# Optimization experiments

Hardware: AMD Instinct MI355X
Metric: run time of the kernel (lower is better)

## Reference

```python
import jax, jax.numpy as jnp
import numpy as np

EMBED_DIM = 512
NUM_HEADS = 8
HEAD_DIM = EMBED_DIM // NUM_HEADS
DECAY = 0.95


def setup_inputs() -> dict:
    key = jax.random.key(0)
    ks = jax.random.split(key, 9)
    B, L, D = 2, 4096, EMBED_DIM
    s = 1.0 / np.sqrt(D)
    inp = {
        "x": jax.random.normal(ks[0], (B, L, D), dtype=jnp.float32),
        "Wq": jax.random.normal(ks[1], (D, D), dtype=jnp.float32) * s,
        "bq": jnp.zeros((D,), jnp.float32),
        "Wk": jax.random.normal(ks[2], (D, D), dtype=jnp.float32) * s,
        "bk": jnp.zeros((D,), jnp.float32),
        "Wv": jax.random.normal(ks[3], (D, D), dtype=jnp.float32) * s,
        "bv": jnp.zeros((D,), jnp.float32),
        "Wo": jax.random.normal(ks[4], (D, D), dtype=jnp.float32) * s,
        "bo": jnp.zeros((D,), jnp.float32),
    }
    return inp


def reference(x, Wq, bq, Wk, bk, Wv, bv, Wo, bo):
    B, L, D = x.shape
    H, Hd = NUM_HEADS, HEAD_DIM
    # temporal decay mask: decay_factor ** |i - j|, shape [L, L]
    idx = jnp.arange(L)
    time_diffs = jnp.abs(idx[None, :] - idx[:, None]).astype(x.dtype)
    decay_mask = jnp.power(jnp.asarray(DECAY, x.dtype), time_diffs)  # [L, L]

    def proj(W, b):
        return (x @ W.T + b).reshape(B, L, H, Hd).transpose(0, 2, 1, 3)  # [B,H,L,Hd]

    q = proj(Wq, bq)
    k = proj(Wk, bk)
    v = proj(Wv, bv)

    scale = 1.0 / np.sqrt(Hd)
    scores = jnp.einsum("bhqd,bhkd->bhqk", q, k) * scale  # [B,H,L,L]
    scores = scores * decay_mask  # broadcast over B, H
    probs = jax.nn.softmax(scores, axis=-1)
    out = jnp.einsum("bhqk,bhkd->bhqd", probs, v)  # [B,H,L,Hd]
    out = out.transpose(0, 2, 1, 3).reshape(B, L, D)
    return out @ Wo.T + bo
```

## Files before the change

### kernel.cpp

```cpp
#include <hip/hip_runtime.h>
#include <hip/hip_bf16.h>

#define L_SEQ 4096
#define NB 2
#define NH 8
#define DHEAD 64
#define DMODEL 512
#define MROWS 8192
#define NTILES 64
#define KWT 2

typedef __attribute__((ext_vector_type(8))) short bf16x8;
typedef __attribute__((ext_vector_type(4))) float f32x4;

#define LOG2_DECAY (-0.07400058144377693f)
#define LOG2E 1.4426950408889634f
#define C_SE (0.125f * LOG2E)
#define C_M8 (-8.0f * LOG2E)
#define EM8 3.3546262790251185e-4f

__device__ __forceinline__ unsigned short f2b(float f) {
    __hip_bfloat16 h = __float2bfloat16(f);
    return *reinterpret_cast<unsigned short*>(&h);
}
__device__ __forceinline__ float b2f(unsigned short u) {
    unsigned int x = ((unsigned int)u) << 16;
    return *reinterpret_cast<float*>(&x);
}
__device__ __forceinline__ void load_lds16(const void* g, void* l) {
    __builtin_amdgcn_global_load_lds(
        (const __attribute__((address_space(1))) unsigned int*)g,
        (__attribute__((address_space(3))) unsigned int*)l, 16, 0, 0);
}

__global__ void cast_all(const float* __restrict__ x,
                         const float* __restrict__ Wq, const float* __restrict__ Wk,
                         const float* __restrict__ Wv, const float* __restrict__ Wo,
                         unsigned short* __restrict__ xb,
                         unsigned short* __restrict__ wqb, unsigned short* __restrict__ wkb,
                         unsigned short* __restrict__ wvb, unsigned short* __restrict__ wob) {
    const int NX = MROWS * DMODEL;
    const int NW = DMODEL * DMODEL;
    int i4 = (blockIdx.x * blockDim.x + threadIdx.x) * 4;
    const float* s;
    unsigned short* o;
    int off;
    if (i4 < NX) { s = x; o = xb; off = i4; }
    else {
        int j = i4 - NX;
        int w = j >> 18;
        off = j & (NW - 1);
        s = w == 0 ? Wq : w == 1 ? Wk : w == 2 ? Wv : Wo;
        o = w == 0 ? wqb : w == 1 ? wkb : w == 2 ? wvb : wob;
    }
    float4 v = *reinterpret_cast<const float4*>(s + off);
    ushort4 u;
    u.x = f2b(v.x); u.y = f2b(v.y); u.z = f2b(v.z); u.w = f2b(v.w);
    *reinterpret_cast<ushort4*>(o + off) = u;
}

__global__ __launch_bounds__(256, 2) void gemm_qkv(const unsigned short* __restrict__ X,
                                                   const unsigned short* __restrict__ W0,
                                                   const unsigned short* __restrict__ W1,
                                                   const unsigned short* __restrict__ W2,
                                                   const float* __restrict__ b0,
                                                   const float* __restrict__ b1,
                                                   const float* __restrict__ b2,
                                                   unsigned short* __restrict__ oQ,
                                                   unsigned short* __restrict__ oK,
                                                   unsigned short* __restrict__ oV,
                                                   float* __restrict__ TS) {
    __shared__ __align__(64) unsigned char smem[40960];
    unsigned short* As = (unsigned short*)smem;
    const int tid = threadIdx.x;
    const int lane = tid & 63;
    const int wave = tid >> 6;
    const int r16 = lane & 15;
    const int g = lane >> 4;
    const int wr = wave >> 1, wc = wave & 1;
    const int m0 = blockIdx.x * 128;
    const int n0 = blockIdx.y * 64;

    f32x4 acc[3][4][2] = {};
    for (int k0 = 0; k0 < DMODEL; k0 += 64) {
        __syncthreads();
#pragma unroll
        for (int c = 0; c < 10; ++c) {
            int ch = wave * 10 + c;
            const unsigned short* gp;
            unsigned char* lp;
            if (ch < 16) {
                int row = ch * 8 + (lane >> 3);
                gp = X + (size_t)(m0 + row) * DMODEL + k0 + (lane & 7) * 8;
                lp = smem + ch * 1024;
            } else {
                int zz = (ch - 16) >> 3;
                int sub = (ch - 16) & 7;
                int row = sub * 8 + (lane >> 3);
                const unsigned short* W = zz == 0 ? W0 : zz == 1 ? W1 : W2;
                gp = W + (size_t)(n0 + row) * DMODEL + k0 + (lane & 7) * 8;
                lp = smem + 16384 + zz * 8192 + sub * 1024;
            }
            load_lds16(gp, lp);
        }
        __syncthreads();
#pragma unroll
        for (int kk = 0; kk < 2; ++kk) {
            bf16x8 a[4];
#pragma unroll
            for (int i = 0; i < 4; ++i)
                a[i] = *(const bf16x8*)(As + (wr * 64 + i * 16 + r16) * 64 + g * 8 + kk * 32);
#pragma unroll
            for (int zz = 0; zz < 3; ++zz) {
                const unsigned short* Bs = (const unsigned short*)(smem + 16384 + zz * 8192);
#pragma unroll
                for (int j = 0; j < 2; ++j) {
                    bf16x8 bfr = *(const bf16x8*)(Bs + (wc * 32 + j * 16 + r16) * 64 + g * 8 + kk * 32);
#pragma unroll
                    for (int i = 0; i < 4; ++i)
                        acc[zz][i][j] = __builtin_amdgcn_mfma_f32_16x16x32_bf16(a[i], bfr, acc[zz][i][j], 0, 0, 0);
                }
            }
        }
    }

    const int b = m0 >> 12;
    const int l0 = m0 & 4095;
    const int h = (n0 >> 6) & 7;

#pragma unroll
    for (int zz = 0; zz < 2; ++zz) {
        const float* bias = zz == 0 ? b0 : b1;
        unsigned short* outB = zz == 0 ? oQ : oK;
#pragma unroll
        for (int i = 0; i < 4; ++i)
#pragma unroll
            for (int j = 0; j < 2; ++j)
#pragma unroll
                for (int r = 0; r < 4; ++r) {
                    int m = m0 + wr * 64 + i * 16 + g * 4 + r;
                    int n = n0 + wc * 32 + j * 16 + r16;
                    float v = acc[zz][i][j][r] + bias[n];
                    int l = m & 4095, hd = n & 63;
                    outB[((size_t)(b * NH + h) * L_SEQ + l) * DHEAD + hd] = f2b(v);
                }
    }

    __syncthreads();
    unsigned short* xsT = (unsigned short*)smem;
#pragma unroll
    for (int i = 0; i < 4; ++i)
#pragma unroll
        for (int j = 0; j < 2; ++j)
#pragma unroll
            for (int r = 0; r < 4; ++r) {
                int nl = wc * 32 + j * 16 + r16;
                int ml = wr * 64 + i * 16 + g * 4 + r;
                xsT[nl * 136 + ml] = f2b(acc[2][i][j][r] + b2[n0 + nl]);
            }
    __syncthreads();
    {
        int drow = tid >> 2, part = tid & 3;
        size_t vb = ((size_t)((b * NH + h) * DHEAD + drow)) * L_SEQ + l0 + part * 32;
#pragma unroll
        for (int e = 0; e < 4; ++e)
            *reinterpret_cast<int4*>(oV + vb + e * 8) =
                *reinterpret_cast<const int4*>(&xsT[drow * 136 + part * 32 + e * 8]);
    }
    if (tid < 128) {
        int d = tid & 63, half = tid >> 6;
        float s = 0.f;
#pragma unroll
        for (int jj = 0; jj < 64; jj += 8) {
            bf16x8 v8 = *reinterpret_cast<const bf16x8*>(&xsT[d * 136 + half * 64 + jj]);
#pragma unroll
            for (int e = 0; e < 8; ++e) s += b2f((unsigned short)v8[e]);
        }
        TS[((size_t)(b * NH + h) * NTILES + (l0 >> 6) + half) * 64 + d] = s;
    }
}

__global__ __launch_bounds__(256) void gemm_out(const unsigned short* __restrict__ X,
                                                const unsigned short* __restrict__ W,
                                                const float* __restrict__ bias,
                                                float* __restrict__ outF) {
    __shared__ __align__(64) unsigned char smem[24576];
    unsigned short* As = (unsigned short*)smem;
    unsigned short* Bs = (unsigned short*)(smem + 16384);
    const int tid = threadIdx.x;
    const int lane = tid & 63;
    const int wave = tid >> 6;
    const int r16 = lane & 15;
    const int g = lane >> 4;
    const int wr = wave >> 1, wc = wave & 1;
    const int m0 = blockIdx.x * 128;
    const int n0 = blockIdx.y * 64;

    f32x4 acc[4][2] = {};
    for (int k0 = 0; k0 < DMODEL; k0 += 64) {
        __syncthreads();
#pragma unroll
        for (int c = 0; c < 6; ++c) {
            int ch = wave * 6 + c;
            const unsigned short* gp;
            unsigned char* lp;
            if (ch < 16) {
                int row = ch * 8 + (lane >> 3);
                gp = X + (size_t)(m0 + row) * DMODEL + k0 + (lane & 7) * 8;
                lp = smem + ch * 1024;
            } else {
                int row = (ch - 16) * 8 + (lane >> 3);
                gp = W + (size_t)(n0 + row) * DMODEL + k0 + (lane & 7) * 8;
                lp = smem + 16384 + (ch - 16) * 1024;
            }
            load_lds16(gp, lp);
        }
        __syncthreads();
#pragma unroll
        for (int kk = 0; kk < 2; ++kk) {
            bf16x8 bfr[2];
#pragma unroll
            for (int j = 0; j < 2; ++j)
                bfr[j] = *(const bf16x8*)(Bs + (wc * 32 + j * 16 + r16) * 64 + g * 8 + kk * 32);
#pragma unroll
            for (int i = 0; i < 4; ++i) {
                bf16x8 a = *(const bf16x8*)(As + (wr * 64 + i * 16 + r16) * 64 + g * 8 + kk * 32);
#pragma unroll
                for (int j = 0; j < 2; ++j)
                    acc[i][j] = __builtin_amdgcn_mfma_f32_16x16x32_bf16(a, bfr[j], acc[i][j], 0, 0, 0);
            }
        }
    }
#pragma unroll
    for (int i = 0; i < 4; ++i)
#pragma unroll
        for (int j = 0; j < 2; ++j)
#pragma unroll
            for (int r = 0; r < 4; ++r) {
                int m = m0 + wr * 64 + i * 16 + g * 4 + r;
                int n = n0 + wc * 32 + j * 16 + r16;
                outF[(size_t)m * DMODEL + n] = acc[i][j][r] + bias[n];
            }
}

__global__ __launch_bounds__(256) void attn_fused(const unsigned short* __restrict__ Qg,
                                                  const unsigned short* __restrict__ Kg,
                                                  const unsigned short* __restrict__ Vtg,
                                                  const float* __restrict__ TS,
                                                  unsigned short* __restrict__ Og) {
    __shared__ __align__(16) unsigned short ks[64][72];
    __shared__ __align__(16) unsigned short vt[64][72];
    __shared__ __align__(16) unsigned short ps[4][32][72];
    __shared__ float Fp[4][64];
    __shared__ float Ftot[64];
    __shared__ float Fband[2][64];
    const int tid = threadIdx.x;
    const int lane = tid & 63;
    const int wave = tid >> 6;
    const int r16 = lane & 15;
    const int g = lane >> 4;
    const int bh = blockIdx.y;
    const int qb = blockIdx.x;
    const int q0 = qb * 128;
    const int qt0 = qb * 2, qt1 = qt0 + 1;
    const size_t base = (size_t)bh * L_SEQ * DHEAD;
    const unsigned short* Qb = Qg + base;
    const unsigned short* Kb = Kg + base;
    const unsigned short* Vtb = Vtg + base;

    const int qtw = qt0 + (wave >> 1);
    const int t_lo_w = (qtw - KWT) > 0 ? (qtw - KWT) : 0;
    const int t_hi_w = (qtw + KWT + 1) < NTILES ? (qtw + KWT + 1) : NTILES;
    const int t_lo_u = (qt0 - KWT) > 0 ? (qt0 - KWT) : 0;
    const int t_hi_u = (qt1 + KWT + 1) < NTILES ? (qt1 + KWT + 1) : NTILES;

    bf16x8 qa[2][2];
#pragma unroll
    for (int f = 0; f < 2; ++f) {
        const unsigned short* qp = Qb + (size_t)(q0 + wave * 32 + f * 16 + r16) * DHEAD + 8 * g;
        qa[f][0] = *reinterpret_cast<const bf16x8*>(qp);
        qa[f][1] = *reinterpret_cast<const bf16x8*>(qp + 32);
    }

    float rowf[2][4], rowfI[2][4], colf[4], colfI[4];
#pragma unroll
    for (int f = 0; f < 2; ++f)
#pragma unroll
        for (int r = 0; r < 4; ++r) {
            float dq = (float)(wave * 32 + f * 16 + g * 4 + r);
            rowf[f][r] = exp2f(dq * LOG2_DECAY);
            rowfI[f][r] = exp2f(-dq * LOG2_DECAY);
        }
#pragma unroll
    for (int t = 0; t < 4; ++t) {
        float dk = (float)(t * 16 + r16);
        colf[t] = exp2f(dk * LOG2_DECAY);
        colfI[t] = exp2f(-dk * LOG2_DECAY);
    }
    float s0f = C_SE * exp2f((float)(q0 - 64 * t_lo_u) * LOG2_DECAY);
    float s0b = C_SE * exp2f(-(float)(q0 - 64 * t_lo_u) * LOG2_DECAY);
    const float stepF = exp2f(-64.f * LOG2_DECAY);
    const float stepB = exp2f(64.f * LOG2_DECAY);

    f32x4 acc[2][4] = {};
    float lpart[2][4] = {};

    const int srow = tid >> 2;
    const int scol = (tid & 3) * 16;
    int4 kr0, kr1, vr0, vr1;
#define ISSUE(KT) { \
    const unsigned short* kp = Kb + ((size_t)((KT) * 64 + srow)) * DHEAD + scol; \
    kr0 = *(const int4*)kp; kr1 = *(const int4*)(kp + 8); \
    const unsigned short* vp = Vtb + (size_t)srow * L_SEQ + (KT) * 64 + scol; \
    vr0 = *(const int4*)vp; vr1 = *(const int4*)(vp + 8); }

    ISSUE(t_lo_u);
    for (int kt = t_lo_u; kt < t_hi_u; ++kt) {
        *(int4*)&ks[srow][scol] = kr0;
        *(int4*)&ks[srow][scol + 8] = kr1;
        *(int4*)&vt[srow][scol] = vr0;
        *(int4*)&vt[srow][scol + 8] = vr1;
        __syncthreads();
        if (kt + 1 < t_hi_u) ISSUE(kt + 1);

        if (kt >= t_lo_w && kt < t_hi_w) {
            f32x4 sc[2][4];
            __builtin_amdgcn_s_setprio(1);
#pragma unroll
            for (int t = 0; t < 4; ++t) {
                bf16x8 b0 = *reinterpret_cast<const bf16x8*>(&ks[t * 16 + r16][8 * g]);
                bf16x8 b1 = *reinterpret_cast<const bf16x8*>(&ks[t * 16 + r16][8 * g + 32]);
#pragma unroll
                for (int f = 0; f < 2; ++f) {
                    f32x4 z = {};
                    z = __builtin_amdgcn_mfma_f32_16x16x32_bf16(qa[f][0], b0, z, 0, 0, 0);
                    z = __builtin_amdgcn_mfma_f32_16x16x32_bf16(qa[f][1], b1, z, 0, 0, 0);
                    sc[f][t] = z;
                }
            }
            __builtin_amdgcn_s_setprio(0);

#pragma unroll
            for (int f = 0; f < 2; ++f) {
                float faf[4], fab[4];
#pragma unroll
                for (int r = 0; r < 4; ++r) {
                    faf[r] = s0f * rowf[f][r];
                    fab[r] = s0b * rowfI[f][r];
                }
#pragma unroll
                for (int t = 0; t < 4; ++t) {
#pragma unroll
                    for (int r = 0; r < 4; ++r) {
                        float mask_se = fminf(faf[r] * colfI[t], fab[r] * colf[t]);
                        float p = exp2f(fmaf(sc[f][t][r], mask_se, C_M8));
                        lpart[f][r] += p;
                        ps[wave][f * 16 + g * 4 + r][t * 16 + r16] = f2b(p);
                    }
                }
            }
            __builtin_amdgcn_s_setprio(1);
#pragma unroll
            for (int f = 0; f < 2; ++f)
#pragma unroll
                for (int t = 0; t < 4; ++t) {
#pragma unroll
                    for (int kk0 = 0; kk0 < 64; kk0 += 32) {
                        bf16x8 pa = *reinterpret_cast<const bf16x8*>(&ps[wave][f * 16 + r16][8 * g + kk0]);
                        bf16x8 vb = *reinterpret_cast<const bf16x8*>(&vt[t * 16 + r16][8 * g + kk0]);
                        acc[f][t] = __builtin_amdgcn_mfma_f32_16x16x32_bf16(pa, vb, acc[f][t], 0, 0, 0);
                    }
                }
            __builtin_amdgcn_s_setprio(0);
        }
        s0f *= stepF;
        s0b *= stepB;
        __syncthreads();
    }
#undef ISSUE

    const float* tsb = TS + (size_t)bh * NTILES * 64;
    {
        int d = tid & 63, c = tid >> 6;
        float f = 0.f;
        for (int t = c; t < NTILES; t += 4) f += tsb[t * 64 + d];
        Fp[c][d] = f;
    }
    __syncthreads();
    if (tid < 64) Ftot[tid] = Fp[0][tid] + Fp[1][tid] + Fp[2][tid] + Fp[3][tid];
    if (tid < 128) {
        int d = tid & 63, which = tid >> 6;
        int qt = which ? qt1 : qt0;
        int tl = (qt - KWT) > 0 ? (qt - KWT) : 0;
        int th = (qt + KWT + 1) < NTILES ? (qt + KWT + 1) : NTILES;
        float s = 0.f;
        for (int t = tl; t < th; ++t) s += tsb[t * 64 + d];
        Fband[which][d] = s;
    }
    __syncthreads();

#pragma unroll
    for (int f = 0; f < 2; ++f)
#pragma unroll
        for (int r = 0; r < 4; ++r) {
#pragma unroll
            for (int sh = 1; sh < 16; sh <<= 1)
                lpart[f][r] += __shfl_xor(lpart[f][r], sh);
        }

    const int whichw = wave >> 1;
    const int nfar = L_SEQ - 64 * (t_hi_w - t_lo_w);
    const int b = bh >> 3, h = bh & 7;
#pragma unroll
    for (int f = 0; f < 2; ++f) {
        float inv[4];
#pragma unroll
        for (int r = 0; r < 4; ++r)
            inv[r] = 1.0f / (lpart[f][r] + EM8 * (float)nfar);
#pragma unroll
        for (int t = 0; t < 4; ++t) {
            float F = Ftot[t * 16 + r16] - Fband[whichw][t * 16 + r16];
#pragma unroll
            for (int r = 0; r < 4; ++r) {
                int row = q0 + wave * 32 + f * 16 + g * 4 + r;
                float o = (acc[f][t][r] + EM8 * F) * inv[r];
                Og[((size_t)(b * L_SEQ) + row) * DMODEL + h * DHEAD + t * 16 + r16] = f2b(o);
            }
        }
    }
}

extern "C" void kernel_launch(void* const* d_in, const int* in_sizes, int n_in,
                              void* d_out, int out_size, void* d_ws, size_t ws_size,
                              hipStream_t stream) {
    const float* x  = (const float*)d_in[0];
    const float* Wq = (const float*)d_in[1];
    const float* bq = (const float*)d_in[2];
    const float* Wk = (const float*)d_in[3];
    const float* bk = (const float*)d_in[4];
    const float* Wv = (const float*)d_in[5];
    const float* bv = (const float*)d_in[6];
    const float* Wo = (const float*)d_in[7];
    const float* bo = (const float*)d_in[8];
    float* out = (float*)d_out;

    const int NX = MROWS * DMODEL;
    const int NW = DMODEL * DMODEL;

    unsigned short* xb  = (unsigned short*)d_ws;
    unsigned short* wqb = xb + NX;
    unsigned short* wkb = wqb + NW;
    unsigned short* wvb = wkb + NW;
    unsigned short* wob = wvb + NW;
    unsigned short* qws = wob + NW;
    unsigned short* kws = qws + NX;
    unsigned short* vtg = kws + NX;
    float* TS = (float*)(vtg + NX);

    const int totalCast = (NX + 4 * NW) / 4;
    cast_all<<<totalCast / 256, 256, 0, stream>>>(x, Wq, Wk, Wv, Wo, xb, wqb, wkb, wvb, wob);

    dim3 gq(MROWS / 128, DMODEL / 64);
    gemm_qkv<<<gq, 256, 0, stream>>>(xb, wqb, wkb, wvb, bq, bk, bv, qws, kws, vtg, TS);

    dim3 ga(L_SEQ / 128, NB * NH);
    attn_fused<<<ga, 256, 0, stream>>>(qws, kws, vtg, TS, xb);

    dim3 go(MROWS / 128, DMODEL / 64);
    gemm_out<<<go, 256, 0, stream>>>(xb, wob, bo, out);
}
```

Measured before the change: 72.06 us.

## Fuse x bf16 cast into QKV GEMM, use hardware bf16/exp instructions

Removes the separate x-to-bf16 cast pass: gemm_qkv now loads fp32 x directly into registers, converts with packed v_cvt_pk_bf16_f32, and writes to LDS, with next-tile prefetch and setprio around the MFMAs. Weight cast and all bf16 stores use the packed hardware conversion instead of the software rounding helper. In attention, exp2f is replaced by raw v_exp_f32 and Q/TS prologue work is reordered to overlap with the first K/V fetch. This saves a full read/write of x in bf16, at the cost of doubling the global traffic for A tiles in the GEMM and adding register pressure.

```diff
diff --git a/kernel.cpp b/kernel.cpp
--- a/kernel.cpp
+++ b/kernel.cpp
@@ -27,39 +27,42 @@
     unsigned int x = ((unsigned int)u) << 16;
     return *reinterpret_cast<float*>(&x);
 }
+__device__ __forceinline__ unsigned cvtpk_bf16(float lo, float hi) {
+    unsigned r;
+    asm("v_cvt_pk_bf16_f32 %0, %1, %2" : "=v"(r) : "v"(lo), "v"(hi));
+    return r;
+}
+__device__ __forceinline__ unsigned short f2b_fast(float f) {
+    return (unsigned short)(cvtpk_bf16(f, f) & 0xffffu);
+}
+__device__ __forceinline__ float fast_exp2(float x) {
+    float r;
+    asm("v_exp_f32 %0, %1" : "=v"(r) : "v"(x));
+    return r;
+}
 __device__ __forceinline__ void load_lds16(const void* g, void* l) {
     __builtin_amdgcn_global_load_lds(
         (const __attribute__((address_space(1))) unsigned int*)g,
         (__attribute__((address_space(3))) unsigned int*)l, 16, 0, 0);
 }
 
-__global__ void cast_all(const float* __restrict__ x,
-                         const float* __restrict__ Wq, const float* __restrict__ Wk,
-                         const float* __restrict__ Wv, const float* __restrict__ Wo,
-                         unsigned short* __restrict__ xb,
-                         unsigned short* __restrict__ wqb, unsigned short* __restrict__ wkb,
-                         unsigned short* __restrict__ wvb, unsigned short* __restrict__ wob) {
-    const int NX = MROWS * DMODEL;
+__global__ void cast_w(const float* __restrict__ Wq, const float* __restrict__ Wk,
+                       const float* __restrict__ Wv, const float* __restrict__ Wo,
+                       unsigned short* __restrict__ wqb, unsigned short* __restrict__ wkb,
+                       unsigned short* __restrict__ wvb, unsigned short* __restrict__ wob) {
     const int NW = DMODEL * DMODEL;
     int i4 = (blockIdx.x * blockDim.x + threadIdx.x) * 4;
-    const float* s;
-    unsigned short* o;
-    int off;
-    if (i4 < NX) { s = x; o = xb; off = i4; }
-    else {
-        int j = i4 - NX;
-        int w = j >> 18;
-        off = j & (NW - 1);
-        s = w == 0 ? Wq : w == 1 ? Wk : w == 2 ? Wv : Wo;
-        o = w == 0 ? wqb : w == 1 ? wkb : w == 2 ? wvb : wob;
-    }
+    int w = i4 >> 18;
+    int off = i4 & (NW - 1);
+    const float* s = w == 0 ? Wq : w == 1 ? Wk : w == 2 ? Wv : Wo;
+    unsigned short* o = w == 0 ? wqb : w == 1 ? wkb : w == 2 ? wvb : wob;
     float4 v = *reinterpret_cast<const float4*>(s + off);
-    ushort4 u;
-    u.x = f2b(v.x); u.y = f2b(v.y); u.z = f2b(v.z); u.w = f2b(v.w);
-    *reinterpret_cast<ushort4*>(o + off) = u;
-}
-
-__global__ __launch_bounds__(256, 2) void gemm_qkv(const unsigned short* __restrict__ X,
+    unsigned lo = cvtpk_bf16(v.x, v.y);
+    unsigned hi = cvtpk_bf16(v.z, v.w);
+    *reinterpret_cast<uint2*>(o + off) = make_uint2(lo, hi);
+}
+
+__global__ __launch_bounds__(256, 2) void gemm_qkv(const float* __restrict__ Xf,
                                                    const unsigned short* __restrict__ W0,
                                                    const unsigned short* __restrict__ W1,
                                                    const unsigned short* __restrict__ W2,
@@ -81,29 +84,43 @@
     const int m0 = blockIdx.x * 128;
     const int n0 = blockIdx.y * 64;
 
+    const int arow = tid >> 3;
+    const int acol = (tid & 7) * 8;
+
+    float4 va[4][2];
+#define ISSUE_A(K0) { \
+    _Pragma("unroll") \
+    for (int j = 0; j < 4; ++j) { \
+        const float* xp = Xf + (size_t)(m0 + arow + j * 32) * DMODEL + (K0) + acol; \
+        va[j][0] = *(const float4*)xp; \
+        va[j][1] = *(const float4*)(xp + 4); \
+    } }
+
     f32x4 acc[3][4][2] = {};
-    for (int k0 = 0; k0 < DMODEL; k0 += 64) {
-        __syncthreads();
-#pragma unroll
-        for (int c = 0; c < 10; ++c) {
-            int ch = wave * 10 + c;
-            const unsigned short* gp;
-            unsigned char* lp;
-            if (ch < 16) {
-                int row = ch * 8 + (lane >> 3);
-                gp = X + (size_t)(m0 + row) * DMODEL + k0 + (lane & 7) * 8;
-                lp = smem + ch * 1024;
-            } else {
-                int zz = (ch - 16) >> 3;
-                int sub = (ch - 16) & 7;
-                int row = sub * 8 + (lane >> 3);
-                const unsigned short* W = zz == 0 ? W0 : zz == 1 ? W1 : W2;
-                gp = W + (size_t)(n0 + row) * DMODEL + k0 + (lane & 7) * 8;
-                lp = smem + 16384 + zz * 8192 + sub * 1024;
-            }
-            load_lds16(gp, lp);
-        }
-        __syncthreads();
+    ISSUE_A(0);
+    for (int s = 0; s < 8; ++s) {
+#pragma unroll
+        for (int j = 0; j < 4; ++j) {
+            unsigned w0 = cvtpk_bf16(va[j][0].x, va[j][0].y);
+            unsigned w1 = cvtpk_bf16(va[j][0].z, va[j][0].w);
+            unsigned w2 = cvtpk_bf16(va[j][1].x, va[j][1].y);
+            unsigned w3 = cvtpk_bf16(va[j][1].z, va[j][1].w);
+            *reinterpret_cast<int4*>(As + (size_t)(arow + j * 32) * 64 + acol) =
+                make_int4(w0, w1, w2, w3);
+        }
+#pragma unroll
+        for (int c = 0; c < 6; ++c) {
+            int ch = wave * 6 + c;
+            int zz = ch >> 3;
+            int sub = ch & 7;
+            int row = sub * 8 + (lane >> 3);
+            const unsigned short* W = zz == 0 ? W0 : zz == 1 ? W1 : W2;
+            load_lds16(W + (size_t)(n0 + row) * DMODEL + s * 64 + (lane & 7) * 8,
+                       smem + 16384 + zz * 8192 + sub * 1024);
+        }
+        __syncthreads();
+        if (s < 7) ISSUE_A((s + 1) * 64);
+        __builtin_amdgcn_s_setprio(1);
 #pragma unroll
         for (int kk = 0; kk < 2; ++kk) {
             bf16x8 a[4];
@@ -122,7 +139,10 @@
                 }
             }
         }
-    }
+        __builtin_amdgcn_s_setprio(0);
+        __syncthreads();
+    }
+#undef ISSUE_A
 
     const int b = m0 >> 12;
     const int l0 = m0 & 4095;
@@ -142,7 +162,7 @@
                     int n = n0 + wc * 32 + j * 16 + r16;
                     float v = acc[zz][i][j][r] + bias[n];
                     int l = m & 4095, hd = n & 63;
-                    outB[((size_t)(b * NH + h) * L_SEQ + l) * DHEAD + hd] = f2b(v);
+                    outB[((size_t)(b * NH + h) * L_SEQ + l) * DHEAD + hd] = f2b_fast(v);
                 }
     }
 
@@ -156,7 +176,7 @@
             for (int r = 0; r < 4; ++r) {
                 int nl = wc * 32 + j * 16 + r16;
                 int ml = wr * 64 + i * 16 + g * 4 + r;
-                xsT[nl * 136 + ml] = f2b(acc[2][i][j][r] + b2[n0 + nl]);
+                xsT[nl * 136 + ml] = f2b_fast(acc[2][i][j][r] + b2[n0 + nl]);
             }
     __syncthreads();
     {
@@ -274,37 +294,6 @@
     const int t_lo_u = (qt0 - KWT) > 0 ? (qt0 - KWT) : 0;
     const int t_hi_u = (qt1 + KWT + 1) < NTILES ? (qt1 + KWT + 1) : NTILES;
 
-    bf16x8 qa[2][2];
-#pragma unroll
-    for (int f = 0; f < 2; ++f) {
-        const unsigned short* qp = Qb + (size_t)(q0 + wave * 32 + f * 16 + r16) * DHEAD + 8 * g;
-        qa[f][0] = *reinterpret_cast<const bf16x8*>(qp);
-        qa[f][1] = *reinterpret_cast<const bf16x8*>(qp + 32);
-    }
-
-    float rowf[2][4], rowfI[2][4], colf[4], colfI[4];
-#pragma unroll
-    for (int f = 0; f < 2; ++f)
-#pragma unroll
-        for (int r = 0; r < 4; ++r) {
-            float dq = (float)(wave * 32 + f * 16 + g * 4 + r);
-            rowf[f][r] = exp2f(dq * LOG2_DECAY);
-            rowfI[f][r] = exp2f(-dq * LOG2_DECAY);
-        }
-#pragma unroll
-    for (int t = 0; t < 4; ++t) {
-        float dk = (float)(t * 16 + r16);
-        colf[t] = exp2f(dk * LOG2_DECAY);
-        colfI[t] = exp2f(-dk * LOG2_DECAY);
-    }
-    float s0f = C_SE * exp2f((float)(q0 - 64 * t_lo_u) * LOG2_DECAY);
-    float s0b = C_SE * exp2f(-(float)(q0 - 64 * t_lo_u) * LOG2_DECAY);
-    const float stepF = exp2f(-64.f * LOG2_DECAY);
-    const float stepB = exp2f(64.f * LOG2_DECAY);
-
-    f32x4 acc[2][4] = {};
-    float lpart[2][4] = {};
-
     const int srow = tid >> 2;
     const int scol = (tid & 3) * 16;
     int4 kr0, kr1, vr0, vr1;
@@ -313,71 +302,15 @@
     kr0 = *(const int4*)kp; kr1 = *(const int4*)(kp + 8); \
     const unsigned short* vp = Vtb + (size_t)srow * L_SEQ + (KT) * 64 + scol; \
     vr0 = *(const int4*)vp; vr1 = *(const int4*)(vp + 8); }
-
     ISSUE(t_lo_u);
-    for (int kt = t_lo_u; kt < t_hi_u; ++kt) {
-        *(int4*)&ks[srow][scol] = kr0;
-        *(int4*)&ks[srow][scol + 8] = kr1;
-        *(int4*)&vt[srow][scol] = vr0;
-        *(int4*)&vt[srow][scol + 8] = vr1;
-        __syncthreads();
-        if (kt + 1 < t_hi_u) ISSUE(kt + 1);
-
-        if (kt >= t_lo_w && kt < t_hi_w) {
-            f32x4 sc[2][4];
-            __builtin_amdgcn_s_setprio(1);
-#pragma unroll
-            for (int t = 0; t < 4; ++t) {
-                bf16x8 b0 = *reinterpret_cast<const bf16x8*>(&ks[t * 16 + r16][8 * g]);
-                bf16x8 b1 = *reinterpret_cast<const bf16x8*>(&ks[t * 16 + r16][8 * g + 32]);
-#pragma unroll
-                for (int f = 0; f < 2; ++f) {
-                    f32x4 z = {};
-                    z = __builtin_amdgcn_mfma_f32_16x16x32_bf16(qa[f][0], b0, z, 0, 0, 0);
-                    z = __builtin_amdgcn_mfma_f32_16x16x32_bf16(qa[f][1], b1, z, 0, 0, 0);
-                    sc[f][t] = z;
-                }
-            }
-            __builtin_amdgcn_s_setprio(0);
-
-#pragma unroll
-            for (int f = 0; f < 2; ++f) {
-                float faf[4], fab[4];
-#pragma unroll
-                for (int r = 0; r < 4; ++r) {
-                    faf[r] = s0f * rowf[f][r];
-                    fab[r] = s0b * rowfI[f][r];
-                }
-#pragma unroll
-                for (int t = 0; t < 4; ++t) {
-#pragma unroll
-                    for (int r = 0; r < 4; ++r) {
-                        float mask_se = fminf(faf[r] * colfI[t], fab[r] * colf[t]);
-                        float p = exp2f(fmaf(sc[f][t][r], mask_se, C_M8));
-                        lpart[f][r] += p;
-                        ps[wave][f * 16 + g * 4 + r][t * 16 + r16] = f2b(p);
-                    }
-                }
-            }
-            __builtin_amdgcn_s_setprio(1);
-#pragma unroll
-            for (int f = 0; f < 2; ++f)
-#pragma unroll
-                for (int t = 0; t < 4; ++t) {
-#pragma unroll
-                    for (int kk0 = 0; kk0 < 64; kk0 += 32) {
-                        bf16x8 pa = *reinterpret_cast<const bf16x8*>(&ps[wave][f * 16 + r16][8 * g + kk0]);
-                        bf16x8 vb = *reinterpret_cast<const bf16x8*>(&vt[t * 16 + r16][8 * g + kk0]);
-                        acc[f][t] = __builtin_amdgcn_mfma_f32_16x16x32_bf16(pa, vb, acc[f][t], 0, 0, 0);
-                    }
-                }
-            __builtin_amdgcn_s_setprio(0);
-        }
-        s0f *= stepF;
-        s0b *= stepB;
-        __syncthreads();
-    }
-#undef ISSUE
+
+    bf16x8 qa[2][2];
+#pragma unroll
+    for (int f = 0; f < 2; ++f) {
+        const unsigned short* qp = Qb + (size_t)(q0 + wave * 32 + f * 16 + r16) * DHEAD + 8 * g;
+        qa[f][0] = *reinterpret_cast<const bf16x8*>(qp);
+        qa[f][1] = *reinterpret_cast<const bf16x8*>(qp + 32);
+    }
 
     const float* tsb = TS + (size_t)bh * NTILES * 64;
     {
@@ -397,7 +330,93 @@
         for (int t = tl; t < th; ++t) s += tsb[t * 64 + d];
         Fband[which][d] = s;
     }
-    __syncthreads();
+
+    float rowf[2][4], rowfI[2][4], colf[4], colfI[4];
+#pragma unroll
+    for (int f = 0; f < 2; ++f)
+#pragma unroll
+        for (int r = 0; r < 4; ++r) {
+            float dq = (float)(wave * 32 + f * 16 + g * 4 + r);
+            rowf[f][r] = fast_exp2(dq * LOG2_DECAY);
+            rowfI[f][r] = fast_exp2(-dq * LOG2_DECAY);
+        }
+#pragma unroll
+    for (int t = 0; t < 4; ++t) {
+        float dk = (float)(t * 16 + r16);
+        colf[t] = fast_exp2(dk * LOG2_DECAY);
+        colfI[t] = fast_exp2(-dk * LOG2_DECAY);
+    }
+    float s0f = C_SE * fast_exp2((float)(q0 - 64 * t_lo_u) * LOG2_DECAY);
+    float s0b = C_SE * fast_exp2(-(float)(q0 - 64 * t_lo_u) * LOG2_DECAY);
+    const float stepF = fast_exp2(-64.f * LOG2_DECAY);
+    const float stepB = fast_exp2(64.f * LOG2_DECAY);
+
+    f32x4 acc[2][4] = {};
+    float lpart[2][4] = {};
+
+    for (int kt = t_lo_u; kt < t_hi_u; ++kt) {
+        *(int4*)&ks[srow][scol] = kr0;
+        *(int4*)&ks[srow][scol + 8] = kr1;
+        *(int4*)&vt[srow][scol] = vr0;
+        *(int4*)&vt[srow][scol + 8] = vr1;
+        __syncthreads();
+        if (kt + 1 < t_hi_u) ISSUE(kt + 1);
+
+        if (kt >= t_lo_w && kt < t_hi_w) {
+            f32x4 sc[2][4];
+            __builtin_amdgcn_s_setprio(1);
+#pragma unroll
+            for (int t = 0; t < 4; ++t) {
+                bf16x8 b0 = *reinterpret_cast<const bf16x8*>(&ks[t * 16 + r16][8 * g]);
+                bf16x8 b1 = *reinterpret_cast<const bf16x8*>(&ks[t * 16 + r16][8 * g + 32]);
+#pragma unroll
+                for (int f = 0; f < 2; ++f) {
+                    f32x4 z = {};
+                    z = __builtin_amdgcn_mfma_f32_16x16x32_bf16(qa[f][0], b0, z, 0, 0, 0);
+                    z = __builtin_amdgcn_mfma_f32_16x16x32_bf16(qa[f][1], b1, z, 0, 0, 0);
+                    sc[f][t] = z;
+                }
+            }
+            __builtin_amdgcn_s_setprio(0);
+
+#pragma unroll
+            for (int f = 0; f < 2; ++f) {
+                float faf[4], fab[4];
+#pragma unroll
+                for (int r = 0; r < 4; ++r) {
+                    faf[r] = s0f * rowf[f][r];
+                    fab[r] = s0b * rowfI[f][r];
+                }
+#pragma unroll
+                for (int t = 0; t < 4; ++t) {
+#pragma unroll
+                    for (int r = 0; r < 4; ++r) {
+                        float mask_se = fminf(faf[r] * colfI[t], fab[r] * colf[t]);
+                        float p = fast_exp2(fmaf(sc[f][t][r], mask_se, C_M8));
+                        lpart[f][r] += p;
+                        ps[wave][f * 16 + g * 4 + r][t * 16 + r16] = f2b_fast(p);
+                    }
+                }
+            }
+            __builtin_amdgcn_s_setprio(1);
+#pragma unroll
+            for (int f = 0; f < 2; ++f)
+#pragma unroll
+                for (int t = 0; t < 4; ++t) {
+#pragma unroll
+                    for (int kk0 = 0; kk0 < 64; kk0 += 32) {
+                        bf16x8 pa = *reinterpret_cast<const bf16x8*>(&ps[wave][f * 16 + r16][8 * g + kk0]);
+                        bf16x8 vb = *reinterpret_cast<const bf16x8*>(&vt[t * 16 + r16][8 * g + kk0]);
+                        acc[f][t] = __builtin_amdgcn_mfma_f32_16x16x32_bf16(pa, vb, acc[f][t], 0, 0, 0);
+                    }
+                }
+            __builtin_amdgcn_s_setprio(0);
+        }
+        s0f *= stepF;
+        s0b *= stepB;
+        __syncthreads();
+    }
+#undef ISSUE
 
 #pragma unroll
     for (int f = 0; f < 2; ++f)
@@ -424,7 +443,7 @@
             for (int r = 0; r < 4; ++r) {
                 int row = q0 + wave * 32 + f * 16 + g * 4 + r;
                 float o = (acc[f][t][r] + EM8 * F) * inv[r];
-                Og[((size_t)(b * L_SEQ) + row) * DMODEL + h * DHEAD + t * 16 + r16] = f2b(o);
+                Og[((size_t)(b * L_SEQ) + row) * DMODEL + h * DHEAD + t * 16 + r16] = f2b_fast(o);
             }
         }
     }
@@ -447,8 +466,8 @@
     const int NX = MROWS * DMODEL;
     const int NW = DMODEL * DMODEL;
 
-    unsigned short* xb  = (unsigned short*)d_ws;
-    unsigned short* wqb = xb + NX;
+    unsigned short* aout = (unsigned short*)d_ws;
+    unsigned short* wqb = aout + NX;
     unsigned short* wkb = wqb + NW;
     unsigned short* wvb = wkb + NW;
     unsigned short* wob = wvb + NW;
@@ -457,15 +476,14 @@
     unsigned short* vtg = kws + NX;
     float* TS = (float*)(vtg + NX);
 
-    const int totalCast = (NX + 4 * NW) / 4;
-    cast_all<<<totalCast / 256, 256, 0, stream>>>(x, Wq, Wk, Wv, Wo, xb, wqb, wkb, wvb, wob);
+    cast_w<<<(4 * NW / 4) / 256, 256, 0, stream>>>(Wq, Wk, Wv, Wo, wqb, wkb, wvb, wob);
 
     dim3 gq(MROWS / 128, DMODEL / 64);
-    gemm_qkv<<<gq, 256, 0, stream>>>(xb, wqb, wkb, wvb, bq, bk, bv, qws, kws, vtg, TS);
+    gemm_qkv<<<gq, 256, 0, stream>>>(x, wqb, wkb, wvb, bq, bk, bv, qws, kws, vtg, TS);
 
     dim3 ga(L_SEQ / 128, NB * NH);
-    attn_fused<<<ga, 256, 0, stream>>>(qws, kws, vtg, TS, xb);
+    attn_fused<<<ga, 256, 0, stream>>>(qws, kws, vtg, TS, aout);
 
     dim3 go(MROWS / 128, DMODEL / 64);
-    gemm_out<<<go, 256, 0, stream>>>(xb, wob, bo, out);
-}
+    gemm_out<<<go, 256, 0, stream>>>(aout, wob, bo, out);
+}
```

Measured after the change: 70.68 us. No clear change (-1.9%).
